# Performance work log

Hardware: AMD Instinct MI355X
Metric: run time of the kernel (lower is better)

Reference implementation:

```python
import jax, jax.numpy as jnp
import numpy as np

ENC, STR_H, CELL_H, ATTN = 512, 256, 512, 512
B, L = 64, 1024


def setup_inputs() -> dict:
    key = jax.random.key(0)
    ks = jax.random.split(key, 12)
    s = lambda fan_in: 1.0 / np.sqrt(fan_in)
    return {
        "encoded_features_map": jax.random.normal(ks[0], (B, L, ENC), jnp.float32),
        "structural_hidden_state": jax.random.normal(ks[1], (1, B, STR_H), jnp.float32),
        "cell_content_hidden_state": jax.random.normal(ks[2], (1, B, CELL_H), jnp.float32),
        "W_enc": jax.random.uniform(ks[3], (ENC, ATTN), jnp.float32, -s(ENC), s(ENC)),
        "b_enc": jax.random.uniform(ks[4], (ATTN,), jnp.float32, -s(ENC), s(ENC)),
        "W_str": jax.random.uniform(ks[5], (STR_H, ATTN), jnp.float32, -s(STR_H), s(STR_H)),
        "b_str": jax.random.uniform(ks[6], (ATTN,), jnp.float32, -s(STR_H), s(STR_H)),
        "W_cell": jax.random.uniform(ks[7], (CELL_H, ATTN), jnp.float32, -s(CELL_H), s(CELL_H)),
        "b_cell": jax.random.uniform(ks[8], (ATTN,), jnp.float32, -s(CELL_H), s(CELL_H)),
        "W_comb": jax.random.uniform(ks[9], (ATTN, 1), jnp.float32, -s(ATTN), s(ATTN)),
        "b_comb": jax.random.uniform(ks[10], (1,), jnp.float32, -s(ATTN), s(ATTN)),
    }


def reference(encoded_features_map, structural_hidden_state, cell_content_hidden_state,
              W_enc, b_enc, W_str, b_str, W_cell, b_cell, W_comb, b_comb):
    # [B, L, A] projection of encoder features
    a_enc = jnp.einsum("ble,ea->bla", encoded_features_map, W_enc) + b_enc
    # [B, A] projections of the two hidden states (squeeze layer dim)
    a_str = structural_hidden_state[0] @ W_str + b_str
    a_cell = cell_content_hidden_state[0] @ W_cell + b_cell
    # broadcast add + ReLU + scalar score: [B, L]
    h = jax.nn.relu(a_enc + a_str[:, None, :] + a_cell[:, None, :])
    scores = jnp.einsum("bla,ao->bl", h, W_comb) + b_comb[0]
    weights = jax.nn.softmax(scores, axis=1)  # over sequence dim
    # weighted sum over L -> [B, ENC]
    context = jnp.einsum("bl,ble->be", weights, encoded_features_map)
    return context
```

## Files before the change

### kernel.cpp

```cpp
#include <hip/hip_runtime.h>
#include <stdint.h>

#define ENC_D 512
#define ATTN_D 512
#define STR_D 256
#define CELL_D 512
#define BATCH 64
#define SEQ 1024
#define NROWS (BATCH * SEQ)

typedef __bf16 bf16x8 __attribute__((ext_vector_type(8)));
typedef float f32x4 __attribute__((ext_vector_type(4)));

__device__ __forceinline__ unsigned short f2bf(float f) {
    unsigned int u = __float_as_uint(f);
    u += 0x7fffu + ((u >> 16) & 1u);
    return (unsigned short)(u >> 16);
}

__device__ __forceinline__ void lds_cp16(void* l, const void* g) {
    __builtin_amdgcn_global_load_lds(
        (const __attribute__((address_space(1))) unsigned int*)g,
        (__attribute__((address_space(3))) unsigned int*)l, 16, 0, 0);
}

#define BAR_VM4() asm volatile("s_waitcnt vmcnt(4)\n\ts_barrier" ::: "memory")
#define BAR_VM0() asm volatile("s_waitcnt vmcnt(0)\n\ts_barrier" ::: "memory")

__global__ __launch_bounds__(256) void k_prep(const float* __restrict__ W,
                                              unsigned short* __restrict__ WF,
                                              const float* __restrict__ str,
                                              const float* __restrict__ cell,
                                              const float* __restrict__ Wstr,
                                              const float* __restrict__ Wcell,
                                              float* __restrict__ bpart) {
    __shared__ char smraw[64 * 68 * 2];
    const int bx = blockIdx.x, t = threadIdx.x;

    if (bx < 64) {
        unsigned short* T = (unsigned short*)smraw;
        const int ei = bx >> 3, ni = bx & 7;
        const int e0 = ei * 64, n0 = ni * 64;
#pragma unroll
        for (int i = 0; i < 4; ++i) {
            const int idx = t + i * 256;
            const int r = idx >> 4, c4 = idx & 15;
            const float4 v = *(const float4*)(W + (size_t)(e0 + r) * ATTN_D + n0 + c4 * 4);
            T[(c4 * 4 + 0) * 68 + r] = f2bf(v.x);
            T[(c4 * 4 + 1) * 68 + r] = f2bf(v.y);
            T[(c4 * 4 + 2) * 68 + r] = f2bf(v.z);
            T[(c4 * 4 + 3) * 68 + r] = f2bf(v.w);
        }
        __syncthreads();
#pragma unroll
        for (int i = 0; i < 2; ++i) {
            const int q = t + i * 256;
            const int n = q >> 3, ge = q & 7;
            union { unsigned short s[8]; uint4 u; } o;
#pragma unroll
            for (int j = 0; j < 8; ++j) o.s[j] = T[n * 68 + ge * 8 + j];
            const int ng = n0 + n;
            const int g = ei * 8 + ge;
            const int nt = ng >> 4, c = ng & 15;
            const int ks = g >> 2, quad = g & 3;
            const int gi = nt * 1024 + ks * 64 + quad * 16 + c;
            *(uint4*)(WF + (size_t)gi * 8) = o.u;
        }
    } else {
        float* sj = (float*)smraw;
        float* red = (float*)smraw + 64;
        const int q = bx - 64;
        const int b = q / 12, jq = q - b * 12;
        const float* hvec;
        const float* Wbase;
        if (jq < 4) { hvec = str + b * STR_D + jq * 64;         Wbase = Wstr + (size_t)(jq * 64) * ATTN_D; }
        else        { hvec = cell + b * CELL_D + (jq - 4) * 64; Wbase = Wcell + (size_t)((jq - 4) * 64) * ATTN_D; }
        if (t < 64) sj[t] = hvec[t];
        __syncthreads();
        const int h = t >> 7, a4 = t & 127;
        f32x4 acc = {0.f, 0.f, 0.f, 0.f};
#pragma unroll 8
        for (int i = h * 32; i < h * 32 + 32; ++i) {
            const float s = sj[i];
            const float4 wv = *(const float4*)(Wbase + (size_t)i * ATTN_D + a4 * 4);
            acc[0] += s * wv.x; acc[1] += s * wv.y; acc[2] += s * wv.z; acc[3] += s * wv.w;
        }
        if (h == 1) *(f32x4*)(red + a4 * 4) = acc;
        __syncthreads();
        if (h == 0) {
            const f32x4 o = *(const f32x4*)(red + a4 * 4);
            acc[0] += o[0]; acc[1] += o[1]; acc[2] += o[2]; acc[3] += o[3];
            *(f32x4*)(bpart + (size_t)(jq * BATCH + b) * ATTN_D + a4 * 4) = acc;
        }
    }
}

__global__ __launch_bounds__(512, 1) void k_scores(const float* __restrict__ E,
                                                   const unsigned short* __restrict__ WF,
                                                   const float* __restrict__ bpart,
                                                   const float* __restrict__ b_enc,
                                                   const float* __restrict__ b_str,
                                                   const float* __restrict__ b_cell,
                                                   const float* __restrict__ Wcomb,
                                                   float* __restrict__ ctxp,
                                                   float* __restrict__ stats) {
    __shared__ unsigned short buf[3][16384];
    __shared__ float sbias[512];
    __shared__ float sWc[512];
    __shared__ float sx[256];
    __shared__ float ex[256];
    __shared__ float red[3][512];
    __shared__ float rtmp[8];

    const int tid = threadIdx.x;
    const int r0 = blockIdx.x * 256;
    const int b = blockIdx.x >> 2;
    const int w = tid >> 6, lane = tid & 63;
    const int quad = lane >> 4, c = lane & 15;

#pragma unroll
    for (int p = 0; p < 2; ++p)
#pragma unroll
        for (int i = 0; i < 4; ++i)
            lds_cp16((char*)&buf[p][0] + i * 8192 + tid * 16,
                     (const char*)WF + (size_t)p * 32768 + i * 8192 + tid * 16);

    if (tid < 128) {
        const int a = tid * 4;
        const float4 be = *(const float4*)(b_enc + a);
        const float4 bs = *(const float4*)(b_str + a);
        const float4 bc = *(const float4*)(b_cell + a);
        f32x4 s;
        s[0] = be.x + bs.x + bc.x; s[1] = be.y + bs.y + bc.y;
        s[2] = be.z + bs.z + bc.z; s[3] = be.w + bs.w + bc.w;
#pragma unroll
        for (int jq = 0; jq < 12; ++jq) {
            const float4 p = *(const float4*)(bpart + (size_t)(jq * BATCH + b) * ATTN_D + a);
            s[0] += p.x; s[1] += p.y; s[2] += p.z; s[3] += p.w;
        }
        *(f32x4*)(sbias + a) = s;
        const float4 wcv = *(const float4*)(Wcomb + a);
        f32x4 wc4; wc4[0] = wcv.x; wc4[1] = wcv.y; wc4[2] = wcv.z; wc4[3] = wcv.w;
        *(f32x4*)(sWc + a) = wc4;
    }

    bf16x8 afr[2][16];
#pragma unroll
    for (int m = 0; m < 2; ++m) {
        const float* Ep = E + (size_t)(r0 + w * 32 + m * 16 + c) * ENC_D + quad * 8;
#pragma unroll
        for (int ks = 0; ks < 16; ++ks) {
            const float4 v0 = *(const float4*)(Ep + ks * 32);
            const float4 v1 = *(const float4*)(Ep + ks * 32 + 4);
            union { unsigned short s[8]; bf16x8 v; } u;
            u.s[0] = f2bf(v0.x); u.s[1] = f2bf(v0.y);
            u.s[2] = f2bf(v0.z); u.s[3] = f2bf(v0.w);
            u.s[4] = f2bf(v1.x); u.s[5] = f2bf(v1.y);
            u.s[6] = f2bf(v1.z); u.s[7] = f2bf(v1.w);
            afr[m][ks] = u.v;
        }
    }

    float sc0[4] = {0.f, 0.f, 0.f, 0.f};
    float sc1[4] = {0.f, 0.f, 0.f, 0.f};

    __syncthreads();

    int cbuf = 0, sbuf = 2;
    for (int ch = 0; ch < 16; ++ch) {
        if (ch < 14) {
            const char* gsrc = (const char*)WF + (size_t)(ch + 2) * 32768;
            char* ldst = (char*)&buf[sbuf][0];
#pragma unroll
            for (int i = 0; i < 4; ++i)
                lds_cp16(ldst + i * 8192 + tid * 16, gsrc + i * 8192 + tid * 16);
        }

        const unsigned short* wb = &buf[cbuf][0];
        f32x4 a0e = {0.f,0.f,0.f,0.f}, a0o = {0.f,0.f,0.f,0.f};
        f32x4 a1e = {0.f,0.f,0.f,0.f}, a1o = {0.f,0.f,0.f,0.f};
        f32x4 b0e = {0.f,0.f,0.f,0.f}, b0o = {0.f,0.f,0.f,0.f};
        f32x4 b1e = {0.f,0.f,0.f,0.f}, b1o = {0.f,0.f,0.f,0.f};
#pragma unroll
        for (int ks = 0; ks < 16; ks += 2) {
            const bf16x8 f0 = *(const bf16x8*)(wb + (ks * 64 + lane) * 8);
            const bf16x8 f1 = *(const bf16x8*)(wb + ((ks + 1) * 64 + lane) * 8);
            const bf16x8 g0 = *(const bf16x8*)(wb + 8192 + (ks * 64 + lane) * 8);
            const bf16x8 g1 = *(const bf16x8*)(wb + 8192 + ((ks + 1) * 64 + lane) * 8);
            a0e = __builtin_amdgcn_mfma_f32_16x16x32_bf16(afr[0][ks], f0, a0e, 0, 0, 0);
            a1e = __builtin_amdgcn_mfma_f32_16x16x32_bf16(afr[1][ks], f0, a1e, 0, 0, 0);
            a0o = __builtin_amdgcn_mfma_f32_16x16x32_bf16(afr[0][ks + 1], f1, a0o, 0, 0, 0);
            a1o = __builtin_amdgcn_mfma_f32_16x16x32_bf16(afr[1][ks + 1], f1, a1o, 0, 0, 0);
            b0e = __builtin_amdgcn_mfma_f32_16x16x32_bf16(afr[0][ks], g0, b0e, 0, 0, 0);
            b1e = __builtin_amdgcn_mfma_f32_16x16x32_bf16(afr[1][ks], g0, b1e, 0, 0, 0);
            b0o = __builtin_amdgcn_mfma_f32_16x16x32_bf16(afr[0][ks + 1], g1, b0o, 0, 0, 0);
            b1o = __builtin_amdgcn_mfma_f32_16x16x32_bf16(afr[1][ks + 1], g1, b1o, 0, 0, 0);
        }

        const int n0 = ch * 32 + c;
        const float bi0 = sbias[n0], wc0 = sWc[n0];
        const float bi1 = sbias[n0 + 16], wc1 = sWc[n0 + 16];
#pragma unroll
        for (int r = 0; r < 4; ++r) {
            float v;
            v = (a0e[r] + a0o[r]) + bi0; sc0[r] += (v > 0.f ? v : 0.f) * wc0;
            v = (b0e[r] + b0o[r]) + bi1; sc0[r] += (v > 0.f ? v : 0.f) * wc1;
            v = (a1e[r] + a1o[r]) + bi0; sc1[r] += (v > 0.f ? v : 0.f) * wc0;
            v = (b1e[r] + b1o[r]) + bi1; sc1[r] += (v > 0.f ? v : 0.f) * wc1;
        }

        cbuf = (cbuf == 2) ? 0 : cbuf + 1;
        sbuf = (sbuf == 2) ? 0 : sbuf + 1;
        if (ch < 15) {
            if (ch < 14) BAR_VM4();
            else         BAR_VM0();
        }
    }

#pragma unroll
    for (int r = 0; r < 4; ++r) {
        float v0 = sc0[r], v1 = sc1[r];
        v0 += __shfl_xor(v0, 1); v1 += __shfl_xor(v1, 1);
        v0 += __shfl_xor(v0, 2); v1 += __shfl_xor(v1, 2);
        v0 += __shfl_xor(v0, 4); v1 += __shfl_xor(v1, 4);
        sc0[r] = v0 + __shfl_xor(v0, 8);
        sc1[r] = v1 + __shfl_xor(v1, 8);
    }
    if (c == 0) {
        const int l0 = w * 32 + quad * 4;
#pragma unroll
        for (int r = 0; r < 4; ++r) sx[l0 + r] = sc0[r];
#pragma unroll
        for (int r = 0; r < 4; ++r) sx[l0 + 16 + r] = sc1[r];
    }
    __syncthreads();

    if (tid < 256) {
        float v = sx[tid];
        float mm = v;
#pragma unroll
        for (int o = 32; o > 0; o >>= 1) mm = fmaxf(mm, __shfl_xor(mm, o));
        if (lane == 0) rtmp[w] = mm;
    }
    __syncthreads();
    const float m_p = fmaxf(fmaxf(rtmp[0], rtmp[1]), fmaxf(rtmp[2], rtmp[3]));
    if (tid < 256) {
        const float e = __expf(sx[tid] - m_p);
        ex[tid] = e;
        float ss = e;
#pragma unroll
        for (int o = 32; o > 0; o >>= 1) ss += __shfl_xor(ss, o);
        if (lane == 0) rtmp[4 + w] = ss;
    }
    __syncthreads();
    if (tid == 0) {
        stats[blockIdx.x * 2 + 0] = m_p;
        stats[blockIdx.x * 2 + 1] = rtmp[4] + rtmp[5] + rtmp[6] + rtmp[7];
    }

    {
        const int g = tid >> 7, col4 = tid & 127;
        const float* Ep = E + (size_t)(r0 + g * 64) * ENC_D + col4 * 4;
        f32x4 acc = {0.f, 0.f, 0.f, 0.f};
#pragma unroll 8
        for (int l = 0; l < 64; ++l) {
            const float4 e4 = *(const float4*)(Ep + (size_t)l * ENC_D);
            const float wgt = ex[g * 64 + l];
            acc[0] += wgt * e4.x; acc[1] += wgt * e4.y;
            acc[2] += wgt * e4.z; acc[3] += wgt * e4.w;
        }
        if (g > 0) *(f32x4*)(&red[g - 1][col4 * 4]) = acc;
        __syncthreads();
        if (g == 0) {
            const f32x4 r1 = *(const f32x4*)(&red[0][col4 * 4]);
            const f32x4 r2 = *(const f32x4*)(&red[1][col4 * 4]);
            const f32x4 r3 = *(const f32x4*)(&red[2][col4 * 4]);
            acc[0] += r1[0] + r2[0] + r3[0];
            acc[1] += r1[1] + r2[1] + r3[1];
            acc[2] += r1[2] + r2[2] + r3[2];
            acc[3] += r1[3] + r2[3] + r3[3];
            *(f32x4*)(ctxp + (size_t)blockIdx.x * 512 + col4 * 4) = acc;
        }
    }
}

__global__ __launch_bounds__(128) void k_final(const float* __restrict__ ctxp,
                                               const float* __restrict__ stats,
                                               float* __restrict__ out) {
    const int b = blockIdx.x, t = threadIdx.x;
    const float m0 = stats[(b * 4 + 0) * 2], z0 = stats[(b * 4 + 0) * 2 + 1];
    const float m1 = stats[(b * 4 + 1) * 2], z1 = stats[(b * 4 + 1) * 2 + 1];
    const float m2 = stats[(b * 4 + 2) * 2], z2 = stats[(b * 4 + 2) * 2 + 1];
    const float m3 = stats[(b * 4 + 3) * 2], z3 = stats[(b * 4 + 3) * 2 + 1];
    const float m = fmaxf(fmaxf(m0, m1), fmaxf(m2, m3));
    const float a0 = __expf(m0 - m), a1 = __expf(m1 - m);
    const float a2 = __expf(m2 - m), a3 = __expf(m3 - m);
    const float invD = 1.f / (z0 * a0 + z1 * a1 + z2 * a2 + z3 * a3);

    const float4 c0 = *(const float4*)(ctxp + (size_t)(b * 4 + 0) * 512 + t * 4);
    const float4 c1 = *(const float4*)(ctxp + (size_t)(b * 4 + 1) * 512 + t * 4);
    const float4 c2 = *(const float4*)(ctxp + (size_t)(b * 4 + 2) * 512 + t * 4);
    const float4 c3 = *(const float4*)(ctxp + (size_t)(b * 4 + 3) * 512 + t * 4);
    f32x4 o;
    o[0] = (c0.x * a0 + c1.x * a1 + c2.x * a2 + c3.x * a3) * invD;
    o[1] = (c0.y * a0 + c1.y * a1 + c2.y * a2 + c3.y * a3) * invD;
    o[2] = (c0.z * a0 + c1.z * a1 + c2.z * a2 + c3.z * a3) * invD;
    o[3] = (c0.w * a0 + c1.w * a1 + c2.w * a2 + c3.w * a3) * invD;
    *(f32x4*)(out + (size_t)b * ENC_D + t * 4) = o;
}

extern "C" void kernel_launch(void* const* d_in, const int* in_sizes, int n_in,
                              void* d_out, int out_size, void* d_ws, size_t ws_size,
                              hipStream_t stream) {
    const float* E      = (const float*)d_in[0];
    const float* str    = (const float*)d_in[1];
    const float* cell   = (const float*)d_in[2];
    const float* Wenc   = (const float*)d_in[3];
    const float* b_enc  = (const float*)d_in[4];
    const float* Wstr   = (const float*)d_in[5];
    const float* b_str  = (const float*)d_in[6];
    const float* Wcell  = (const float*)d_in[7];
    const float* b_cell = (const float*)d_in[8];
    const float* Wcomb  = (const float*)d_in[9];
    float* out = (float*)d_out;

    char* ws = (char*)d_ws;
    unsigned short* WF = (unsigned short*)ws;
    float* bpart = (float*)(ws + (512 << 10));
    float* ctxp  = (float*)(ws + (512 << 10) + (1536 << 10));
    float* stats = (float*)(ws + (512 << 10) + (2048 << 10));

    k_prep<<<832, 256, 0, stream>>>(Wenc, WF, str, cell, Wstr, Wcell, bpart);
    k_scores<<<NROWS / 256, 512, 0, stream>>>(E, WF, bpart, b_enc, b_str, b_cell, Wcomb, ctxp, stats);
    k_final<<<BATCH, 128, 0, stream>>>(ctxp, stats, out);
}
```

Measured before the change: 270.0 us.

## Retile score GEMM to K-chunk streaming with 128-row blocks and 2D warp split

Restructures the score kernel so each block handles 128 rows instead of 256. Warps are arranged as a 2x4 grid over rows and attention columns. The weight layout is reordered so each LDS chunk holds a K-slice covering all 512 output columns, and E is streamed per K-chunk instead of preloaded whole into registers. Accumulators stay resident across all chunks and bias/ReLU/score reduction run once at the end, with a cross-warp reduction via LDS. This doubles the grid, targets 2 blocks per CU and reduces per-thread A-fragment register use. The trade-off is a larger 128-float accumulator per thread, more partial softmax stats to merge in the final kernel, and possible LDS limits on occupancy.

```diff
diff --git a/kernel.cpp b/kernel.cpp
--- a/kernel.cpp
+++ b/kernel.cpp
@@ -25,7 +25,6 @@
 }
 
 #define BAR_VM4() asm volatile("s_waitcnt vmcnt(4)\n\ts_barrier" ::: "memory")
-#define BAR_VM0() asm volatile("s_waitcnt vmcnt(0)\n\ts_barrier" ::: "memory")
 
 __global__ __launch_bounds__(256) void k_prep(const float* __restrict__ W,
                                               unsigned short* __restrict__ WF,
@@ -63,7 +62,7 @@
             const int g = ei * 8 + ge;
             const int nt = ng >> 4, c = ng & 15;
             const int ks = g >> 2, quad = g & 3;
-            const int gi = nt * 1024 + ks * 64 + quad * 16 + c;
+            const int gi = ks * 2048 + nt * 64 + quad * 16 + c;
             *(uint4*)(WF + (size_t)gi * 8) = o.u;
         }
     } else {
@@ -95,7 +94,7 @@
     }
 }
 
-__global__ __launch_bounds__(512, 1) void k_scores(const float* __restrict__ E,
+__global__ __launch_bounds__(512, 2) void k_scores(const float* __restrict__ E,
                                                    const unsigned short* __restrict__ WF,
                                                    const float* __restrict__ bpart,
                                                    const float* __restrict__ b_enc,
@@ -107,15 +106,17 @@
     __shared__ unsigned short buf[3][16384];
     __shared__ float sbias[512];
     __shared__ float sWc[512];
-    __shared__ float sx[256];
-    __shared__ float ex[256];
+    __shared__ float sxp[4][128];
+    __shared__ float sx[128];
+    __shared__ float ex[128];
     __shared__ float red[3][512];
-    __shared__ float rtmp[8];
+    __shared__ float rtmp[4];
 
     const int tid = threadIdx.x;
-    const int r0 = blockIdx.x * 256;
-    const int b = blockIdx.x >> 2;
+    const int r0 = blockIdx.x * 128;
+    const int b = blockIdx.x >> 3;
     const int w = tid >> 6, lane = tid & 63;
+    const int wm = w >> 2, wn = w & 3;
     const int quad = lane >> 4, c = lane & 15;
 
 #pragma unroll
@@ -144,30 +145,29 @@
         *(f32x4*)(sWc + a) = wc4;
     }
 
-    bf16x8 afr[2][16];
-#pragma unroll
-    for (int m = 0; m < 2; ++m) {
-        const float* Ep = E + (size_t)(r0 + w * 32 + m * 16 + c) * ENC_D + quad * 8;
-#pragma unroll
-        for (int ks = 0; ks < 16; ++ks) {
-            const float4 v0 = *(const float4*)(Ep + ks * 32);
-            const float4 v1 = *(const float4*)(Ep + ks * 32 + 4);
-            union { unsigned short s[8]; bf16x8 v; } u;
-            u.s[0] = f2bf(v0.x); u.s[1] = f2bf(v0.y);
-            u.s[2] = f2bf(v0.z); u.s[3] = f2bf(v0.w);
-            u.s[4] = f2bf(v1.x); u.s[5] = f2bf(v1.y);
-            u.s[6] = f2bf(v1.z); u.s[7] = f2bf(v1.w);
-            afr[m][ks] = u.v;
-        }
-    }
-
-    float sc0[4] = {0.f, 0.f, 0.f, 0.f};
-    float sc1[4] = {0.f, 0.f, 0.f, 0.f};
+    f32x4 acc[4][8];
+#pragma unroll
+    for (int mt = 0; mt < 4; ++mt)
+#pragma unroll
+        for (int nt = 0; nt < 8; ++nt) {
+            const f32x4 z = {0.f, 0.f, 0.f, 0.f};
+            acc[mt][nt] = z;
+        }
 
     __syncthreads();
+
+    const float* Ebase = E + (size_t)(r0 + wm * 64 + c) * ENC_D + quad * 8;
 
     int cbuf = 0, sbuf = 2;
     for (int ch = 0; ch < 16; ++ch) {
+        float4 v0[4], v1[4];
+#pragma unroll
+        for (int mt = 0; mt < 4; ++mt) {
+            const float* Ep = Ebase + (size_t)(mt * 16) * ENC_D + ch * 32;
+            v0[mt] = *(const float4*)(Ep);
+            v1[mt] = *(const float4*)(Ep + 4);
+        }
+
         if (ch < 14) {
             const char* gsrc = (const char*)WF + (size_t)(ch + 2) * 32768;
             char* ldst = (char*)&buf[sbuf][0];
@@ -176,110 +176,117 @@
                 lds_cp16(ldst + i * 8192 + tid * 16, gsrc + i * 8192 + tid * 16);
         }
 
+        bf16x8 av[4];
+#pragma unroll
+        for (int mt = 0; mt < 4; ++mt) {
+            union { unsigned short s[8]; bf16x8 v; } u;
+            u.s[0] = f2bf(v0[mt].x); u.s[1] = f2bf(v0[mt].y);
+            u.s[2] = f2bf(v0[mt].z); u.s[3] = f2bf(v0[mt].w);
+            u.s[4] = f2bf(v1[mt].x); u.s[5] = f2bf(v1[mt].y);
+            u.s[6] = f2bf(v1[mt].z); u.s[7] = f2bf(v1[mt].w);
+            av[mt] = u.v;
+        }
+
         const unsigned short* wb = &buf[cbuf][0];
-        f32x4 a0e = {0.f,0.f,0.f,0.f}, a0o = {0.f,0.f,0.f,0.f};
-        f32x4 a1e = {0.f,0.f,0.f,0.f}, a1o = {0.f,0.f,0.f,0.f};
-        f32x4 b0e = {0.f,0.f,0.f,0.f}, b0o = {0.f,0.f,0.f,0.f};
-        f32x4 b1e = {0.f,0.f,0.f,0.f}, b1o = {0.f,0.f,0.f,0.f};
-#pragma unroll
-        for (int ks = 0; ks < 16; ks += 2) {
-            const bf16x8 f0 = *(const bf16x8*)(wb + (ks * 64 + lane) * 8);
-            const bf16x8 f1 = *(const bf16x8*)(wb + ((ks + 1) * 64 + lane) * 8);
-            const bf16x8 g0 = *(const bf16x8*)(wb + 8192 + (ks * 64 + lane) * 8);
-            const bf16x8 g1 = *(const bf16x8*)(wb + 8192 + ((ks + 1) * 64 + lane) * 8);
-            a0e = __builtin_amdgcn_mfma_f32_16x16x32_bf16(afr[0][ks], f0, a0e, 0, 0, 0);
-            a1e = __builtin_amdgcn_mfma_f32_16x16x32_bf16(afr[1][ks], f0, a1e, 0, 0, 0);
-            a0o = __builtin_amdgcn_mfma_f32_16x16x32_bf16(afr[0][ks + 1], f1, a0o, 0, 0, 0);
-            a1o = __builtin_amdgcn_mfma_f32_16x16x32_bf16(afr[1][ks + 1], f1, a1o, 0, 0, 0);
-            b0e = __builtin_amdgcn_mfma_f32_16x16x32_bf16(afr[0][ks], g0, b0e, 0, 0, 0);
-            b1e = __builtin_amdgcn_mfma_f32_16x16x32_bf16(afr[1][ks], g0, b1e, 0, 0, 0);
-            b0o = __builtin_amdgcn_mfma_f32_16x16x32_bf16(afr[0][ks + 1], g1, b0o, 0, 0, 0);
-            b1o = __builtin_amdgcn_mfma_f32_16x16x32_bf16(afr[1][ks + 1], g1, b1o, 0, 0, 0);
-        }
-
-        const int n0 = ch * 32 + c;
-        const float bi0 = sbias[n0], wc0 = sWc[n0];
-        const float bi1 = sbias[n0 + 16], wc1 = sWc[n0 + 16];
-#pragma unroll
-        for (int r = 0; r < 4; ++r) {
-            float v;
-            v = (a0e[r] + a0o[r]) + bi0; sc0[r] += (v > 0.f ? v : 0.f) * wc0;
-            v = (b0e[r] + b0o[r]) + bi1; sc0[r] += (v > 0.f ? v : 0.f) * wc1;
-            v = (a1e[r] + a1o[r]) + bi0; sc1[r] += (v > 0.f ? v : 0.f) * wc0;
-            v = (b1e[r] + b1o[r]) + bi1; sc1[r] += (v > 0.f ? v : 0.f) * wc1;
-        }
+        bf16x8 bfr[8];
+#pragma unroll
+        for (int nt = 0; nt < 8; ++nt)
+            bfr[nt] = *(const bf16x8*)(wb + ((wn * 8 + nt) * 64 + lane) * 8);
+#pragma unroll
+        for (int nt = 0; nt < 8; ++nt)
+#pragma unroll
+            for (int mt = 0; mt < 4; ++mt)
+                acc[mt][nt] = __builtin_amdgcn_mfma_f32_16x16x32_bf16(av[mt], bfr[nt], acc[mt][nt], 0, 0, 0);
 
         cbuf = (cbuf == 2) ? 0 : cbuf + 1;
         sbuf = (sbuf == 2) ? 0 : sbuf + 1;
-        if (ch < 15) {
-            if (ch < 14) BAR_VM4();
-            else         BAR_VM0();
-        }
-    }
-
-#pragma unroll
-    for (int r = 0; r < 4; ++r) {
-        float v0 = sc0[r], v1 = sc1[r];
-        v0 += __shfl_xor(v0, 1); v1 += __shfl_xor(v1, 1);
-        v0 += __shfl_xor(v0, 2); v1 += __shfl_xor(v1, 2);
-        v0 += __shfl_xor(v0, 4); v1 += __shfl_xor(v1, 4);
-        sc0[r] = v0 + __shfl_xor(v0, 8);
-        sc1[r] = v1 + __shfl_xor(v1, 8);
-    }
+        if (ch < 15) BAR_VM4();
+    }
+
+    float sp[4][4];
+#pragma unroll
+    for (int mt = 0; mt < 4; ++mt)
+#pragma unroll
+        for (int reg = 0; reg < 4; ++reg) sp[mt][reg] = 0.f;
+#pragma unroll
+    for (int nt = 0; nt < 8; ++nt) {
+        const int col = wn * 128 + nt * 16 + c;
+        const float bi = sbias[col], wc = sWc[col];
+#pragma unroll
+        for (int mt = 0; mt < 4; ++mt)
+#pragma unroll
+            for (int reg = 0; reg < 4; ++reg) {
+                const float v = acc[mt][nt][reg] + bi;
+                sp[mt][reg] += (v > 0.f ? v : 0.f) * wc;
+            }
+    }
+#pragma unroll
+    for (int mt = 0; mt < 4; ++mt)
+#pragma unroll
+        for (int reg = 0; reg < 4; ++reg) {
+            float v = sp[mt][reg];
+            v += __shfl_xor(v, 1);
+            v += __shfl_xor(v, 2);
+            v += __shfl_xor(v, 4);
+            v += __shfl_xor(v, 8);
+            sp[mt][reg] = v;
+        }
     if (c == 0) {
-        const int l0 = w * 32 + quad * 4;
-#pragma unroll
-        for (int r = 0; r < 4; ++r) sx[l0 + r] = sc0[r];
-#pragma unroll
-        for (int r = 0; r < 4; ++r) sx[l0 + 16 + r] = sc1[r];
+#pragma unroll
+        for (int mt = 0; mt < 4; ++mt)
+#pragma unroll
+            for (int reg = 0; reg < 4; ++reg)
+                sxp[wn][wm * 64 + mt * 16 + quad * 4 + reg] = sp[mt][reg];
     }
     __syncthreads();
 
-    if (tid < 256) {
-        float v = sx[tid];
-        float mm = v;
+    if (tid < 128)
+        sx[tid] = sxp[0][tid] + sxp[1][tid] + sxp[2][tid] + sxp[3][tid];
+
+    if (tid < 128) {
+        float mm = sx[tid];
 #pragma unroll
         for (int o = 32; o > 0; o >>= 1) mm = fmaxf(mm, __shfl_xor(mm, o));
         if (lane == 0) rtmp[w] = mm;
     }
     __syncthreads();
-    const float m_p = fmaxf(fmaxf(rtmp[0], rtmp[1]), fmaxf(rtmp[2], rtmp[3]));
-    if (tid < 256) {
+    const float m_p = fmaxf(rtmp[0], rtmp[1]);
+    if (tid < 128) {
         const float e = __expf(sx[tid] - m_p);
         ex[tid] = e;
         float ss = e;
 #pragma unroll
         for (int o = 32; o > 0; o >>= 1) ss += __shfl_xor(ss, o);
-        if (lane == 0) rtmp[4 + w] = ss;
+        if (lane == 0) rtmp[2 + w] = ss;
     }
     __syncthreads();
     if (tid == 0) {
         stats[blockIdx.x * 2 + 0] = m_p;
-        stats[blockIdx.x * 2 + 1] = rtmp[4] + rtmp[5] + rtmp[6] + rtmp[7];
+        stats[blockIdx.x * 2 + 1] = rtmp[2] + rtmp[3];
     }
 
     {
         const int g = tid >> 7, col4 = tid & 127;
-        const float* Ep = E + (size_t)(r0 + g * 64) * ENC_D + col4 * 4;
-        f32x4 acc = {0.f, 0.f, 0.f, 0.f};
+        const float* Ep = E + (size_t)(r0 + g * 32) * ENC_D + col4 * 4;
+        f32x4 a4 = {0.f, 0.f, 0.f, 0.f};
 #pragma unroll 8
-        for (int l = 0; l < 64; ++l) {
+        for (int l = 0; l < 32; ++l) {
             const float4 e4 = *(const float4*)(Ep + (size_t)l * ENC_D);
-            const float wgt = ex[g * 64 + l];
-            acc[0] += wgt * e4.x; acc[1] += wgt * e4.y;
-            acc[2] += wgt * e4.z; acc[3] += wgt * e4.w;
-        }
-        if (g > 0) *(f32x4*)(&red[g - 1][col4 * 4]) = acc;
+            const float wgt = ex[g * 32 + l];
+            a4[0] += wgt * e4.x; a4[1] += wgt * e4.y;
+            a4[2] += wgt * e4.z; a4[3] += wgt * e4.w;
+        }
+        if (g > 0) *(f32x4*)(&red[g - 1][col4 * 4]) = a4;
         __syncthreads();
         if (g == 0) {
             const f32x4 r1 = *(const f32x4*)(&red[0][col4 * 4]);
             const f32x4 r2 = *(const f32x4*)(&red[1][col4 * 4]);
             const f32x4 r3 = *(const f32x4*)(&red[2][col4 * 4]);
-            acc[0] += r1[0] + r2[0] + r3[0];
-            acc[1] += r1[1] + r2[1] + r3[1];
-            acc[2] += r1[2] + r2[2] + r3[2];
-            acc[3] += r1[3] + r2[3] + r3[3];
-            *(f32x4*)(ctxp + (size_t)blockIdx.x * 512 + col4 * 4) = acc;
+            a4[0] += r1[0] + r2[0] + r3[0];
+            a4[1] += r1[1] + r2[1] + r3[1];
+            a4[2] += r1[2] + r2[2] + r3[2];
+            a4[3] += r1[3] + r2[3] + r3[3];
+            *(f32x4*)(ctxp + (size_t)blockIdx.x * 512 + col4 * 4) = a4;
         }
     }
 }
@@ -288,24 +295,28 @@
                                                const float* __restrict__ stats,
                                                float* __restrict__ out) {
     const int b = blockIdx.x, t = threadIdx.x;
-    const float m0 = stats[(b * 4 + 0) * 2], z0 = stats[(b * 4 + 0) * 2 + 1];
-    const float m1 = stats[(b * 4 + 1) * 2], z1 = stats[(b * 4 + 1) * 2 + 1];
-    const float m2 = stats[(b * 4 + 2) * 2], z2 = stats[(b * 4 + 2) * 2 + 1];
-    const float m3 = stats[(b * 4 + 3) * 2], z3 = stats[(b * 4 + 3) * 2 + 1];
-    const float m = fmaxf(fmaxf(m0, m1), fmaxf(m2, m3));
-    const float a0 = __expf(m0 - m), a1 = __expf(m1 - m);
-    const float a2 = __expf(m2 - m), a3 = __expf(m3 - m);
-    const float invD = 1.f / (z0 * a0 + z1 * a1 + z2 * a2 + z3 * a3);
-
-    const float4 c0 = *(const float4*)(ctxp + (size_t)(b * 4 + 0) * 512 + t * 4);
-    const float4 c1 = *(const float4*)(ctxp + (size_t)(b * 4 + 1) * 512 + t * 4);
-    const float4 c2 = *(const float4*)(ctxp + (size_t)(b * 4 + 2) * 512 + t * 4);
-    const float4 c3 = *(const float4*)(ctxp + (size_t)(b * 4 + 3) * 512 + t * 4);
-    f32x4 o;
-    o[0] = (c0.x * a0 + c1.x * a1 + c2.x * a2 + c3.x * a3) * invD;
-    o[1] = (c0.y * a0 + c1.y * a1 + c2.y * a2 + c3.y * a3) * invD;
-    o[2] = (c0.z * a0 + c1.z * a1 + c2.z * a2 + c3.z * a3) * invD;
-    o[3] = (c0.w * a0 + c1.w * a1 + c2.w * a2 + c3.w * a3) * invD;
+    float mp[8], zp[8];
+    float m = -1e30f;
+#pragma unroll
+    for (int p = 0; p < 8; ++p) {
+        mp[p] = stats[(b * 8 + p) * 2];
+        zp[p] = stats[(b * 8 + p) * 2 + 1];
+        m = fmaxf(m, mp[p]);
+    }
+    float D = 0.f;
+    float a[8];
+#pragma unroll
+    for (int p = 0; p < 8; ++p) { a[p] = __expf(mp[p] - m); D += zp[p] * a[p]; }
+    const float invD = 1.f / D;
+
+    f32x4 o = {0.f, 0.f, 0.f, 0.f};
+#pragma unroll
+    for (int p = 0; p < 8; ++p) {
+        const float4 cp = *(const float4*)(ctxp + (size_t)(b * 8 + p) * 512 + t * 4);
+        o[0] += cp.x * a[p]; o[1] += cp.y * a[p];
+        o[2] += cp.z * a[p]; o[3] += cp.w * a[p];
+    }
+    o[0] *= invD; o[1] *= invD; o[2] *= invD; o[3] *= invD;
     *(f32x4*)(out + (size_t)b * ENC_D + t * 4) = o;
 }
 
@@ -328,9 +339,9 @@
     unsigned short* WF = (unsigned short*)ws;
     float* bpart = (float*)(ws + (512 << 10));
     float* ctxp  = (float*)(ws + (512 << 10) + (1536 << 10));
-    float* stats = (float*)(ws + (512 << 10) + (2048 << 10));
+    float* stats = (float*)(ws + (512 << 10) + (2560 << 10));
 
     k_prep<<<832, 256, 0, stream>>>(Wenc, WF, str, cell, Wstr, Wcell, bpart);
-    k_scores<<<NROWS / 256, 512, 0, stream>>>(E, WF, bpart, b_enc, b_str, b_cell, Wcomb, ctxp, stats);
+    k_scores<<<NROWS / 128, 512, 0, stream>>>(E, WF, bpart, b_enc, b_str, b_cell, Wcomb, ctxp, stats);
     k_final<<<BATCH, 128, 0, stream>>>(ctxp, stats, out);
 }
```

New measurement: 286.3 us. 1.06x slower.
